# Kernel optimization log

Hardware: AMD Instinct MI355X
Metric: run time of the kernel (lower is better)

The kernel has to match this reference:

```python
import jax, jax.numpy as jnp
import numpy as np

N = 50000
E = 800000
DIMS = [(8, 16), (16, 16), (16, 16)]  # (in, out) per layer


def setup_inputs() -> dict:
    key = jax.random.key(0)
    ks = jax.random.split(key, 32)
    inp = {}
    inp['x'] = jax.random.normal(ks[0], (N, 8), dtype=jnp.float32)
    inp['pos'] = jax.random.normal(ks[1], (N, 3), dtype=jnp.float32)
    k = 2
    for i, (ci, co) in enumerate(DIMS):
        d = ci * co
        inp[f'lin_w{i}'] = jax.random.normal(ks[k], (3, d), dtype=jnp.float32); k += 1
        inp[f'lin_b{i}'] = jax.random.normal(ks[k], (d,), dtype=jnp.float32); k += 1
        inp[f'gamma{i}'] = jax.random.normal(ks[k], (d,), dtype=jnp.float32); k += 1
        inp[f'beta{i}'] = jax.random.normal(ks[k], (d,), dtype=jnp.float32); k += 1
        inp[f'root{i}'] = jax.random.normal(ks[k], (ci, co), dtype=jnp.float32); k += 1
        inp[f'bias{i}'] = jax.random.normal(ks[k], (co,), dtype=jnp.float32); k += 1
    inp['batch'] = jnp.zeros((N,), dtype=jnp.int32)
    inp['idx'] = jnp.sort(jax.random.randint(ks[k], (25000,), 0, N, dtype=jnp.int32)); k += 1
    inp['edge_index'] = jax.random.randint(ks[k], (2, E), 0, N, dtype=jnp.int32)
    return inp


def _nnconv(x, pseudo, src, dst, lin_w, lin_b, gamma, beta, root, bias, ci, co):
    # edge MLP (Linear -> batchnorm(eval, affine) -> ReLU), plain_last=False
    w = jax.nn.relu((pseudo @ lin_w + lin_b) * gamma + beta)  # [E, ci*co]
    w = w.reshape(-1, ci, co)                                  # [E, ci, co]
    msg = jnp.einsum('ei,eio->eo', x[src], w)                  # per-edge vec-mat
    s = jax.ops.segment_sum(msg, dst, num_segments=N)          # scatter-sum
    cnt = jax.ops.segment_sum(jnp.ones((msg.shape[0],), x.dtype), dst, num_segments=N)
    aggr = s / jnp.maximum(cnt, 1.0)[:, None]                  # scatter-mean
    return aggr + x @ root + bias


def reference(x, pos, lin_w0, lin_b0, gamma0, beta0, root0, bias0,
              lin_w1, lin_b1, gamma1, beta1, root1, bias1,
              lin_w2, lin_b2, gamma2, beta2, root2, bias2,
              batch, idx, edge_index):
    src, dst = edge_index[0], edge_index[1]
    pseudo = pos[dst] - pos[src]  # patch_size is None
    params = [
        (lin_w0, lin_b0, gamma0, beta0, root0, bias0),
        (lin_w1, lin_b1, gamma1, beta1, root1, bias1),
        (lin_w2, lin_b2, gamma2, beta2, root2, bias2),
    ]
    h = x
    for (ci, co), p in zip(DIMS, params):
        h = jax.nn.relu(_nnconv(h, pseudo, src, dst, *p, ci, co))  # drop_act=False
    return h[idx], pos[idx], batch[idx]
```

## Files before the change

kernel.cpp:

```cpp
#include <hip/hip_runtime.h>

#define N_NODES 50000
#define N_EDGES 800000
#define M_IDX   25000
#define DMAX    64

__global__ __launch_bounds__(256) void fold_kernel(
    const float* __restrict__ lw0, const float* __restrict__ lb0,
    const float* __restrict__ g0,  const float* __restrict__ b0,
    const float* __restrict__ lw1, const float* __restrict__ lb1,
    const float* __restrict__ g1,  const float* __restrict__ b1,
    const float* __restrict__ lw2, const float* __restrict__ lb2,
    const float* __restrict__ g2,  const float* __restrict__ b2,
    float4* __restrict__ wtab)
{
    const int l = blockIdx.x, j = threadIdx.x;
    const float *lw, *lb, *gm, *bt; int d;
    if (l == 0)      { lw = lw0; lb = lb0; gm = g0; bt = b0; d = 128; }
    else if (l == 1) { lw = lw1; lb = lb1; gm = g1; bt = b1; d = 256; }
    else             { lw = lw2; lb = lb2; gm = g2; bt = b2; d = 256; }
    if (j < d) {
        const float g = gm[j];
        float4 w4;
        w4.x = lw[j] * g;
        w4.y = lw[d + j] * g;
        w4.z = lw[2 * d + j] * g;
        w4.w = fmaf(lb[j], g, bt[j]);
        wtab[l * 256 + j] = w4;
    }
}

__global__ __launch_bounds__(256) void prep_kernel(
    const int*   __restrict__ ei,
    const float* __restrict__ pos,
    int*         __restrict__ cnt,
    float4*      __restrict__ pdata,
    int E)
{
    const int e0 = blockIdx.x * 512 + threadIdx.x;
    const int e1 = e0 + 256;
    const bool v0 = e0 < E, v1 = e1 < E;
    int t0 = 0, s0 = 0, t1 = 0, s1 = 0;
    if (v0) { t0 = ei[E + e0]; s0 = ei[e0]; }
    if (v1) { t1 = ei[E + e1]; s1 = ei[e1]; }
    int p0 = 0, p1 = 0;
    if (v0) p0 = atomicAdd(&cnt[t0], 1);
    if (v1) p1 = atomicAdd(&cnt[t1], 1);
    if (v0) {
        float4 pd;
        pd.x = pos[t0 * 3 + 0] - pos[s0 * 3 + 0];
        pd.y = pos[t0 * 3 + 1] - pos[s0 * 3 + 1];
        pd.z = pos[t0 * 3 + 2] - pos[s0 * 3 + 2];
        pd.w = __int_as_float(s0);
        if (p0 < DMAX) pdata[(size_t)t0 * DMAX + p0] = pd;
    }
    if (v1) {
        float4 pd;
        pd.x = pos[t1 * 3 + 0] - pos[s1 * 3 + 0];
        pd.y = pos[t1 * 3 + 1] - pos[s1 * 3 + 1];
        pd.z = pos[t1 * 3 + 2] - pos[s1 * 3 + 2];
        pd.w = __int_as_float(s1);
        if (p1 < DMAX) pdata[(size_t)t1 * DMAX + p1] = pd;
    }
}

template<int IQ>
__device__ __forceinline__ void load_q(float* dst, const float* src) {
    if constexpr (IQ == 4) {
        float4 v = *(const float4*)src;
        dst[0] = v.x; dst[1] = v.y; dst[2] = v.z; dst[3] = v.w;
    } else {
        float2 v = *(const float2*)src;
        dst[0] = v.x; dst[1] = v.y;
    }
}

template<int CI>
__global__ __launch_bounds__(256) void node_wave_kernel(
    const float4* __restrict__ pdata,
    const int*    __restrict__ cnt,
    const float*  __restrict__ h_in,
    const float4* __restrict__ wt_l,
    const float*  __restrict__ root,
    const float*  __restrict__ bias,
    float*        __restrict__ h_out,
    int N)
{
    constexpr int IQ = CI / 4;
    const int tid  = threadIdx.x;
    const int lane = tid & 63;
    const int eg   = lane >> 4;
    const int o    = lane & 15;
    const int t    = blockIdx.x * 4 + (tid >> 6);

    const float4* __restrict__ wt = wt_l + (eg * IQ) * 16 + o;
    float4 w4[IQ];
#pragma unroll
    for (int z = 0; z < IQ; ++z) w4[z] = wt[z * 16];

    const int deg = cnt[t];
    const int dl  = min(deg, DMAX);
    const float4* __restrict__ row = pdata + (size_t)t * DMAX;
    const float*  __restrict__ xq_base = h_in + eg * IQ;

    float acc = 0.f;
    int p = 0;
    for (; p + 2 <= dl; p += 2) {
        float4 pdA = row[p];
        float4 pdB = row[p + 1];
        const int sA = __float_as_int(pdA.w);
        const int sB = __float_as_int(pdB.w);
        float xA[IQ], xB[IQ];
        load_q<IQ>(xA, xq_base + (size_t)sA * CI);
        load_q<IQ>(xB, xq_base + (size_t)sB * CI);
        float eA = 0.f, eB = 0.f;
#pragma unroll
        for (int z = 0; z < IQ; ++z) {
            float wA = fmaf(pdA.z, w4[z].z, fmaf(pdA.y, w4[z].y, fmaf(pdA.x, w4[z].x, w4[z].w)));
            eA = fmaf(xA[z], fmaxf(wA, 0.f), eA);
            float wB = fmaf(pdB.z, w4[z].z, fmaf(pdB.y, w4[z].y, fmaf(pdB.x, w4[z].x, w4[z].w)));
            eB = fmaf(xB[z], fmaxf(wB, 0.f), eB);
        }
        acc += eA + eB;
    }
    if (p < dl) {
        float4 pdA = row[p];
        const int sA = __float_as_int(pdA.w);
        float xA[IQ];
        load_q<IQ>(xA, xq_base + (size_t)sA * CI);
#pragma unroll
        for (int z = 0; z < IQ; ++z) {
            float wA = fmaf(pdA.z, w4[z].z, fmaf(pdA.y, w4[z].y, fmaf(pdA.x, w4[z].x, w4[z].w)));
            acc = fmaf(xA[z], fmaxf(wA, 0.f), acc);
        }
    }

    float xT[IQ];
    load_q<IQ>(xT, xq_base + (size_t)t * CI);
    float rp = 0.f;
#pragma unroll
    for (int z = 0; z < IQ; ++z)
        rp = fmaf(xT[z], root[(eg * IQ + z) * 16 + o], rp);

    float contrib = fmaf(acc, 1.0f / fmaxf((float)deg, 1.0f), rp);
    contrib += __shfl_xor(contrib, 16);
    contrib += __shfl_xor(contrib, 32);

    if (eg == 0) h_out[t * 16 + o] = fmaxf(contrib + bias[o], 0.f);
}

__global__ __launch_bounds__(256) void gather_kernel(
    const float* __restrict__ h,
    const float* __restrict__ pos,
    const int*   __restrict__ batch,
    const int*   __restrict__ idx,
    float*       __restrict__ out,
    int M)
{
    int j = blockIdx.x * blockDim.x + threadIdx.x;
    if (j >= M) return;
    int n = idx[j];
    float4*       o4 = (float4*)out + (size_t)j * 4;
    const float4* h4 = (const float4*)(h + (size_t)n * 16);
    o4[0] = h4[0]; o4[1] = h4[1]; o4[2] = h4[2]; o4[3] = h4[3];
    float* po = out + (size_t)M * 16 + (size_t)j * 3;
    po[0] = pos[n * 3 + 0];
    po[1] = pos[n * 3 + 1];
    po[2] = pos[n * 3 + 2];
    ((int*)out)[(size_t)M * 19 + j] = batch[n];
}

extern "C" void kernel_launch(void* const* d_in, const int* in_sizes, int n_in,
                              void* d_out, int out_size, void* d_ws, size_t ws_size,
                              hipStream_t stream) {
    const float* x      = (const float*)d_in[0];
    const float* pos    = (const float*)d_in[1];
    const float* lin_w0 = (const float*)d_in[2];
    const float* lin_b0 = (const float*)d_in[3];
    const float* gamma0 = (const float*)d_in[4];
    const float* beta0  = (const float*)d_in[5];
    const float* root0  = (const float*)d_in[6];
    const float* bias0  = (const float*)d_in[7];
    const float* lin_w1 = (const float*)d_in[8];
    const float* lin_b1 = (const float*)d_in[9];
    const float* gamma1 = (const float*)d_in[10];
    const float* beta1  = (const float*)d_in[11];
    const float* root1  = (const float*)d_in[12];
    const float* bias1  = (const float*)d_in[13];
    const float* lin_w2 = (const float*)d_in[14];
    const float* lin_b2 = (const float*)d_in[15];
    const float* gamma2 = (const float*)d_in[16];
    const float* beta2  = (const float*)d_in[17];
    const float* root2  = (const float*)d_in[18];
    const float* bias2  = (const float*)d_in[19];
    const int*   batch  = (const int*)d_in[20];
    const int*   idx    = (const int*)d_in[21];
    const int*   ei     = (const int*)d_in[22];
    float*       out    = (float*)d_out;

    float4* pdata = (float4*)d_ws;
    float*  hA    = (float*)(pdata + (size_t)N_NODES * DMAX);
    float*  hB    = hA + (size_t)N_NODES * 16;
    int*    cnt   = (int*)(hB + (size_t)N_NODES * 16);
    float4* wtab  = (float4*)(cnt + N_NODES);

    hipMemsetAsync(cnt, 0, N_NODES * sizeof(int), stream);
    fold_kernel<<<3, 256, 0, stream>>>(lin_w0, lin_b0, gamma0, beta0,
                                       lin_w1, lin_b1, gamma1, beta1,
                                       lin_w2, lin_b2, gamma2, beta2, wtab);
    prep_kernel<<<(N_EDGES + 511) / 512, 256, 0, stream>>>(ei, pos, cnt, pdata, N_EDGES);

    const int NB = N_NODES / 4;

    node_wave_kernel<8><<<NB, 256, 0, stream>>>(pdata, cnt, x,
        wtab, root0, bias0, hA, N_NODES);
    node_wave_kernel<16><<<NB, 256, 0, stream>>>(pdata, cnt, hA,
        wtab + 256, root1, bias1, hB, N_NODES);
    node_wave_kernel<16><<<NB, 256, 0, stream>>>(pdata, cnt, hB,
        wtab + 512, root2, bias2, hA, N_NODES);

    gather_kernel<<<(M_IDX + 255) / 256, 256, 0, stream>>>(hA, pos, batch, idx, out, M_IDX);
}
```

Before: 329.8 us.

## Fuse weight fold into prep, persistent waves, packed v2f math, prefetch edges

Merges the weight-fold kernel into the edge prep kernel, saving one launch. The node kernel becomes a grid-stride persistent loop over 2048 blocks, so folded weights and root values are loaded into registers once per wave rather than once per node. It also uses 2-wide vector FMAs, which can map to packed fp32 instructions, and software-prefetches the next edge pair. The risks are the tail handling, which now does redundant loads for odd degrees, and possible load imbalance across waves.

```diff
diff --git a/kernel.cpp b/kernel.cpp
--- a/kernel.cpp
+++ b/kernel.cpp
@@ -5,38 +5,39 @@
 #define M_IDX   25000
 #define DMAX    64
 
-__global__ __launch_bounds__(256) void fold_kernel(
+typedef float v2f __attribute__((ext_vector_type(2)));
+
+__global__ __launch_bounds__(256) void prep_kernel(
+    const int*   __restrict__ ei,
+    const float* __restrict__ pos,
+    int*         __restrict__ cnt,
+    float4*      __restrict__ pdata,
     const float* __restrict__ lw0, const float* __restrict__ lb0,
     const float* __restrict__ g0,  const float* __restrict__ b0,
     const float* __restrict__ lw1, const float* __restrict__ lb1,
     const float* __restrict__ g1,  const float* __restrict__ b1,
     const float* __restrict__ lw2, const float* __restrict__ lb2,
     const float* __restrict__ g2,  const float* __restrict__ b2,
-    float4* __restrict__ wtab)
-{
-    const int l = blockIdx.x, j = threadIdx.x;
-    const float *lw, *lb, *gm, *bt; int d;
-    if (l == 0)      { lw = lw0; lb = lb0; gm = g0; bt = b0; d = 128; }
-    else if (l == 1) { lw = lw1; lb = lb1; gm = g1; bt = b1; d = 256; }
-    else             { lw = lw2; lb = lb2; gm = g2; bt = b2; d = 256; }
-    if (j < d) {
-        const float g = gm[j];
-        float4 w4;
-        w4.x = lw[j] * g;
-        w4.y = lw[d + j] * g;
-        w4.z = lw[2 * d + j] * g;
-        w4.w = fmaf(lb[j], g, bt[j]);
-        wtab[l * 256 + j] = w4;
-    }
-}
-
-__global__ __launch_bounds__(256) void prep_kernel(
-    const int*   __restrict__ ei,
-    const float* __restrict__ pos,
-    int*         __restrict__ cnt,
-    float4*      __restrict__ pdata,
+    float4*      __restrict__ wtab,
     int E)
 {
+    if (blockIdx.x < 3) {
+        const int l = blockIdx.x, j = threadIdx.x;
+        const float *lw, *lb, *gm, *bt; int d;
+        if (l == 0)      { lw = lw0; lb = lb0; gm = g0; bt = b0; d = 128; }
+        else if (l == 1) { lw = lw1; lb = lb1; gm = g1; bt = b1; d = 256; }
+        else             { lw = lw2; lb = lb2; gm = g2; bt = b2; d = 256; }
+        if (j < d) {
+            const float g = gm[j];
+            float4 w4;
+            w4.x = lw[j] * g;
+            w4.y = lw[d + j] * g;
+            w4.z = lw[2 * d + j] * g;
+            w4.w = fmaf(lb[j], g, bt[j]);
+            wtab[l * 256 + j] = w4;
+        }
+    }
+
     const int e0 = blockIdx.x * 512 + threadIdx.x;
     const int e1 = e0 + 256;
     const bool v0 = e0 < E, v1 = e1 < E;
@@ -65,13 +66,14 @@
 }
 
 template<int IQ>
-__device__ __forceinline__ void load_q(float* dst, const float* src) {
+__device__ __forceinline__ void load_x(const float* __restrict__ h, int s, int eg, v2f* xv) {
     if constexpr (IQ == 4) {
-        float4 v = *(const float4*)src;
-        dst[0] = v.x; dst[1] = v.y; dst[2] = v.z; dst[3] = v.w;
+        float4 v = ((const float4*)h)[s * 4 + eg];
+        xv[0] = (v2f){v.x, v.y};
+        xv[1] = (v2f){v.z, v.w};
     } else {
-        float2 v = *(const float2*)src;
-        dst[0] = v.x; dst[1] = v.y;
+        float2 v = ((const float2*)h)[s * 4 + eg];
+        xv[0] = (v2f){v.x, v.y};
     }
 }
 
@@ -87,66 +89,80 @@
     int N)
 {
     constexpr int IQ = CI / 4;
-    const int tid  = threadIdx.x;
-    const int lane = tid & 63;
-    const int eg   = lane >> 4;
-    const int o    = lane & 15;
-    const int t    = blockIdx.x * 4 + (tid >> 6);
-
-    const float4* __restrict__ wt = wt_l + (eg * IQ) * 16 + o;
-    float4 w4[IQ];
+    constexpr int NP = IQ / 2;
+    const int gtid   = blockIdx.x * blockDim.x + threadIdx.x;
+    const int wid    = gtid >> 6;
+    const int nwaves = (gridDim.x * blockDim.x) >> 6;
+    const int lane   = gtid & 63;
+    const int eg     = lane >> 4;
+    const int o      = lane & 15;
+
+    v2f W0[NP], W1[NP], W2[NP], Bv[NP], Rv[NP];
 #pragma unroll
-    for (int z = 0; z < IQ; ++z) w4[z] = wt[z * 16];
-
-    const int deg = cnt[t];
-    const int dl  = min(deg, DMAX);
-    const float4* __restrict__ row = pdata + (size_t)t * DMAX;
-    const float*  __restrict__ xq_base = h_in + eg * IQ;
-
-    float acc = 0.f;
-    int p = 0;
-    for (; p + 2 <= dl; p += 2) {
-        float4 pdA = row[p];
-        float4 pdB = row[p + 1];
-        const int sA = __float_as_int(pdA.w);
-        const int sB = __float_as_int(pdB.w);
-        float xA[IQ], xB[IQ];
-        load_q<IQ>(xA, xq_base + (size_t)sA * CI);
-        load_q<IQ>(xB, xq_base + (size_t)sB * CI);
-        float eA = 0.f, eB = 0.f;
+    for (int u = 0; u < NP; ++u) {
+        float4 wa = wt_l[(eg * IQ + 2 * u) * 16 + o];
+        float4 wb = wt_l[(eg * IQ + 2 * u + 1) * 16 + o];
+        W0[u] = (v2f){wa.x, wb.x};
+        W1[u] = (v2f){wa.y, wb.y};
+        W2[u] = (v2f){wa.z, wb.z};
+        Bv[u] = (v2f){wa.w, wb.w};
+        Rv[u] = (v2f){root[(eg * IQ + 2 * u) * 16 + o],
+                      root[(eg * IQ + 2 * u + 1) * 16 + o]};
+    }
+    const float bo = bias[o];
+    const v2f zero = 0.f;
+
+    for (int t = wid; t < N; t += nwaves) {
+        const int deg = cnt[t];
+        const int dl  = min(deg, DMAX);
+        const float4* __restrict__ row = pdata + (size_t)t * DMAX;
+
+        float4 pdA = row[0], pdB = row[1];
+        v2f vacc = 0.f;
+        for (int p = 0; p < dl; p += 2) {
+            const bool okB = (p + 1) < dl;
+            const int sA = __float_as_int(pdA.w);
+            const int sB = okB ? __float_as_int(pdB.w) : sA;
+            v2f xA[NP], xB[NP];
+            load_x<IQ>(h_in, sA, eg, xA);
+            load_x<IQ>(h_in, sB, eg, xB);
+            const int pn = min(p + 2, DMAX - 2);
+            float4 pdA2 = row[pn], pdB2 = row[pn + 1];
+            v2f ax = pdA.x, ay = pdA.y, az = pdA.z;
+            v2f bx = pdB.x, by = pdB.y, bz = pdB.z;
+            v2f eA = 0.f, eB = 0.f;
 #pragma unroll
-        for (int z = 0; z < IQ; ++z) {
-            float wA = fmaf(pdA.z, w4[z].z, fmaf(pdA.y, w4[z].y, fmaf(pdA.x, w4[z].x, w4[z].w)));
-            eA = fmaf(xA[z], fmaxf(wA, 0.f), eA);
-            float wB = fmaf(pdB.z, w4[z].z, fmaf(pdB.y, w4[z].y, fmaf(pdB.x, w4[z].x, w4[z].w)));
-            eB = fmaf(xB[z], fmaxf(wB, 0.f), eB);
+            for (int u = 0; u < NP; ++u) {
+                v2f wA = __builtin_elementwise_fma(az, W2[u],
+                         __builtin_elementwise_fma(ay, W1[u],
+                         __builtin_elementwise_fma(ax, W0[u], Bv[u])));
+                wA = __builtin_elementwise_max(wA, zero);
+                eA = __builtin_elementwise_fma(xA[u], wA, eA);
+                v2f wB = __builtin_elementwise_fma(bz, W2[u],
+                         __builtin_elementwise_fma(by, W1[u],
+                         __builtin_elementwise_fma(bx, W0[u], Bv[u])));
+                wB = __builtin_elementwise_max(wB, zero);
+                eB = __builtin_elementwise_fma(xB[u], wB, eB);
+            }
+            vacc += eA + (okB ? eB : zero);
+            pdA = pdA2; pdB = pdB2;
         }
-        acc += eA + eB;
-    }
-    if (p < dl) {
-        float4 pdA = row[p];
-        const int sA = __float_as_int(pdA.w);
-        float xA[IQ];
-        load_q<IQ>(xA, xq_base + (size_t)sA * CI);
+        float acc = vacc.x + vacc.y;
+
+        v2f xT[NP];
+        load_x<IQ>(h_in, t, eg, xT);
+        v2f rpv = 0.f;
 #pragma unroll
-        for (int z = 0; z < IQ; ++z) {
-            float wA = fmaf(pdA.z, w4[z].z, fmaf(pdA.y, w4[z].y, fmaf(pdA.x, w4[z].x, w4[z].w)));
-            acc = fmaf(xA[z], fmaxf(wA, 0.f), acc);
-        }
-    }
-
-    float xT[IQ];
-    load_q<IQ>(xT, xq_base + (size_t)t * CI);
-    float rp = 0.f;
-#pragma unroll
-    for (int z = 0; z < IQ; ++z)
-        rp = fmaf(xT[z], root[(eg * IQ + z) * 16 + o], rp);
-
-    float contrib = fmaf(acc, 1.0f / fmaxf((float)deg, 1.0f), rp);
-    contrib += __shfl_xor(contrib, 16);
-    contrib += __shfl_xor(contrib, 32);
-
-    if (eg == 0) h_out[t * 16 + o] = fmaxf(contrib + bias[o], 0.f);
+        for (int u = 0; u < NP; ++u)
+            rpv = __builtin_elementwise_fma(xT[u], Rv[u], rpv);
+        float rp = rpv.x + rpv.y;
+
+        float contrib = fmaf(acc, 1.0f / fmaxf((float)deg, 1.0f), rp);
+        contrib += __shfl_xor(contrib, 16);
+        contrib += __shfl_xor(contrib, 32);
+
+        if (eg == 0) h_out[t * 16 + o] = fmaxf(contrib + bo, 0.f);
+    }
 }
 
 __global__ __launch_bounds__(256) void gather_kernel(
@@ -205,12 +221,13 @@
     float4* wtab  = (float4*)(cnt + N_NODES);
 
     hipMemsetAsync(cnt, 0, N_NODES * sizeof(int), stream);
-    fold_kernel<<<3, 256, 0, stream>>>(lin_w0, lin_b0, gamma0, beta0,
-                                       lin_w1, lin_b1, gamma1, beta1,
-                                       lin_w2, lin_b2, gamma2, beta2, wtab);
-    prep_kernel<<<(N_EDGES + 511) / 512, 256, 0, stream>>>(ei, pos, cnt, pdata, N_EDGES);
-
-    const int NB = N_NODES / 4;
+    prep_kernel<<<(N_EDGES + 511) / 512, 256, 0, stream>>>(
+        ei, pos, cnt, pdata,
+        lin_w0, lin_b0, gamma0, beta0,
+        lin_w1, lin_b1, gamma1, beta1,
+        lin_w2, lin_b2, gamma2, beta2, wtab, N_EDGES);
+
+    const int NB = 2048;
 
     node_wave_kernel<8><<<NB, 256, 0, stream>>>(pdata, cnt, x,
         wtab, root0, bias0, hA, N_NODES);
```

Measured after the change: 324.3 us. About the same (-1.7%).
